# Performance work log

Measured on AMD Instinct MI355X. Metric: run time of the kernel, lower is better.

## Reference

```python
import jax, jax.numpy as jnp
import numpy as np

N_NODES = 50000
NEG_SLOPE = 0.2


def gat_conv(x, edge_index, W, a_src, a_dst, b):
    """PyG GATConv, heads=1: linear -> per-edge attention -> segment softmax -> scatter-add."""
    n = x.shape[0]
    h = x @ W                                   # [N, out]
    # add self-loops (PyG default add_self_loops=True)
    loop = jnp.arange(n, dtype=edge_index.dtype)
    src = jnp.concatenate([edge_index[0], loop])  # message sources j
    dst = jnp.concatenate([edge_index[1], loop])  # aggregation targets i
    alpha_s = h @ a_src                          # [N]
    alpha_d = h @ a_dst                          # [N]
    e = jax.nn.leaky_relu(alpha_s[src] + alpha_d[dst], NEG_SLOPE)  # [E+N]
    # numerically stable segment softmax over edges grouped by dst
    m = jax.ops.segment_max(e, dst, num_segments=n)
    ex = jnp.exp(e - m[dst])
    denom = jax.ops.segment_sum(ex, dst, num_segments=n)
    alpha = ex / denom[dst]                      # [E+N]
    out = jax.ops.segment_sum(h[src] * alpha[:, None], dst, num_segments=n)
    return out + b


def setup_inputs() -> dict:
    key = jax.random.key(0)
    ks = jax.random.split(key, 12)
    F_IN, H1, H2 = 128, 64, 32
    E, ED = 800000, 800000
    x = jax.random.normal(ks[0], (N_NODES, F_IN), dtype=jnp.float32)
    edge_index = jax.random.randint(ks[1], (2, E), 0, N_NODES, dtype=jnp.int64)
    pos_edge_index = jax.random.randint(ks[2], (2, ED), 0, N_NODES, dtype=jnp.int64)
    neg_edge_index = jax.random.randint(ks[3], (2, ED), 0, N_NODES, dtype=jnp.int64)
    g = lambda k, shape, fan: (jax.random.normal(k, shape, dtype=jnp.float32) * (1.0 / np.sqrt(fan))).astype(jnp.float32)
    W1 = g(ks[4], (F_IN, H1), F_IN)
    a_src1 = g(ks[5], (H1,), H1)
    a_dst1 = g(ks[6], (H1,), H1)
    b1 = jnp.zeros((H1,), dtype=jnp.float32)
    W2 = g(ks[7], (H1, H2), H1)
    a_src2 = g(ks[8], (H2,), H2)
    a_dst2 = g(ks[9], (H2,), H2)
    b2 = jnp.zeros((H2,), dtype=jnp.float32)
    return {"x": x, "edge_index": edge_index, "pos_edge_index": pos_edge_index,
            "neg_edge_index": neg_edge_index, "W1": W1, "a_src1": a_src1,
            "a_dst1": a_dst1, "b1": b1, "W2": W2, "a_src2": a_src2,
            "a_dst2": a_dst2, "b2": b2}


def reference(x, edge_index, pos_edge_index, neg_edge_index,
              W1, a_src1, a_dst1, b1, W2, a_src2, a_dst2, b2):
    # encode (dropout omitted: eval-mode)
    h = gat_conv(x, edge_index, W1, a_src1, a_dst1, b1)
    h = jax.nn.relu(h)
    z = gat_conv(h, edge_index, W2, a_src2, a_dst2, b2)
    # decode: per-edge dot products on concatenated pos/neg edges
    ei = jnp.concatenate([pos_edge_index, neg_edge_index], axis=-1)
    logits = jnp.sum(z[ei[0]] * z[ei[1]], axis=-1)
    return logits
```

## Files before the change

kernel.cpp:

```cpp
#include <hip/hip_runtime.h>

#define NEG_SLOPE 0.2f

constexpr int N_NODES = 50000;
constexpr int TPB = 256;
constexpr int BSH = 7;
constexpr int NB = (N_NODES + 127) >> BSH;
constexpr int SCAT_CHUNK = 8192;

__device__ __forceinline__ unsigned short f2b(float f) {
  unsigned u = __float_as_uint(f);
  return (unsigned short)((u + 0x7FFFu + ((u >> 16) & 1u)) >> 16);
}
__device__ __forceinline__ float b2f(unsigned short b) {
  return __uint_as_float(((unsigned)b) << 16);
}
__device__ __forceinline__ float blo(unsigned u) {
  return __uint_as_float(u << 16);
}
__device__ __forceinline__ float bhi(unsigned u) {
  return __uint_as_float(u & 0xFFFF0000u);
}
__device__ __forceinline__ unsigned pack2(float a, float b) {
  return (unsigned)f2b(a) | ((unsigned)f2b(b) << 16);
}

__global__ void zero_ints(int* __restrict__ p, int n) {
  int i = blockIdx.x * blockDim.x + threadIdx.x;
  if (i < n) p[i] = 0;
}

__global__ void transpose_w4(const float* __restrict__ W,
                             float4* __restrict__ Wt, int K, int OUTD) {
  int i = blockIdx.x * blockDim.x + threadIdx.x;
  if (i >= (K / 4) * OUTD) return;
  int k4 = i / OUTD, c = i % OUTD;
  Wt[i] = make_float4(W[(4 * k4 + 0) * OUTD + c], W[(4 * k4 + 1) * OUTD + c],
                      W[(4 * k4 + 2) * OUTD + c], W[(4 * k4 + 3) * OUTD + c]);
}

template <int K, int OUTD>
__global__ __launch_bounds__(TPB) void gemm_alpha(
    const float* __restrict__ X, const float4* __restrict__ Wt,
    const float* __restrict__ avec_src, const float* __restrict__ avec_dst,
    unsigned short* __restrict__ Hout, float* __restrict__ as_out,
    float* __restrict__ ad_out, int n) {
  constexpr int BK = 16;
  constexpr int NT = K / BK;
  constexpr int CT = OUTD / 2;
  constexpr int RG = 64 / CT;
  constexpr int RPT = 16 / RG;
  constexpr int WPB = TPB / 64;
  __shared__ float xs[WPB][2][16][BK + 4];

  const int t = threadIdx.x;
  const int wid = t >> 6;
  const int lane = t & 63;
  const int waveRow0 = blockIdx.x * (WPB * 16) + wid * 16;

  const int srow = lane >> 2;
  const int skq = lane & 3;
  const float* srcRow = X + (size_t)min(waveRow0 + srow, n - 1) * K + skq * 4;

  const int cc = lane % CT;
  const int c0 = 2 * cc;
  const int rg = lane / CT;
  const int r0 = rg * RPT;

  const float a_s0 = avec_src[c0], a_s1 = avec_src[c0 + 1];
  const float a_d0 = avec_dst[c0], a_d1 = avec_dst[c0 + 1];

  float4 g = *(const float4*)srcRow;
  *(float4*)&xs[wid][0][srow][skq * 4] = g;

  float acc[RPT][2];
#pragma unroll
  for (int i = 0; i < RPT; ++i) acc[i][0] = acc[i][1] = 0.f;

  for (int tile = 0;;) {
    if (tile + 1 < NT)
      g = *(const float4*)(srcRow + (size_t)(tile + 1) * BK);
    const int buf = tile & 1;
#pragma unroll
    for (int kq = 0; kq < BK / 4; ++kq) {
      const int kqg = tile * (BK / 4) + kq;
      const float4 w0 = Wt[(size_t)kqg * OUTD + c0];
      const float4 w1 = Wt[(size_t)kqg * OUTD + c0 + 1];
#pragma unroll
      for (int i = 0; i < RPT; ++i) {
        const float4 xv = *(const float4*)&xs[wid][buf][r0 + i][kq * 4];
        acc[i][0] = fmaf(xv.x, w0.x, acc[i][0]);
        acc[i][1] = fmaf(xv.x, w1.x, acc[i][1]);
        acc[i][0] = fmaf(xv.y, w0.y, acc[i][0]);
        acc[i][1] = fmaf(xv.y, w1.y, acc[i][1]);
        acc[i][0] = fmaf(xv.z, w0.z, acc[i][0]);
        acc[i][1] = fmaf(xv.z, w1.z, acc[i][1]);
        acc[i][0] = fmaf(xv.w, w0.w, acc[i][0]);
        acc[i][1] = fmaf(xv.w, w1.w, acc[i][1]);
      }
    }
    if (++tile == NT) break;
    *(float4*)&xs[wid][tile & 1][srow][skq * 4] = g;
  }

#pragma unroll
  for (int i = 0; i < RPT; ++i) {
    const int r = waveRow0 + r0 + i;
    if (r < n) {
      ushort2 hb;
      hb.x = f2b(acc[i][0]);
      hb.y = f2b(acc[i][1]);
      ((ushort2*)Hout)[(size_t)r * CT + cc] = hb;
      float vs = acc[i][0] * a_s0 + acc[i][1] * a_s1;
      float vd = acc[i][0] * a_d0 + acc[i][1] * a_d1;
#pragma unroll
      for (int m = CT / 2; m >= 1; m >>= 1) {
        vs += __shfl_xor(vs, m);
        vd += __shfl_xor(vd, m);
      }
      if (cc == 0) {
        as_out[r] = vs;
        ad_out[r] = vd;
      }
    }
  }
}

__global__ void bucket_hist(const int* __restrict__ edst, int E,
                            int* __restrict__ pairCnt) {
  __shared__ int h[NB];
  for (int i = threadIdx.x; i < NB; i += blockDim.x) h[i] = 0;
  __syncthreads();
  for (int i = blockIdx.x * blockDim.x + threadIdx.x; i < E;
       i += gridDim.x * blockDim.x)
    atomicAdd(&h[edst[i] >> BSH], 1);
  __syncthreads();
  for (int i = threadIdx.x; i < NB; i += blockDim.x)
    if (h[i]) atomicAdd(&pairCnt[i], h[i]);
}

__global__ void bucket_scan(const int* __restrict__ pairCnt,
                            int* __restrict__ pairOff,
                            int* __restrict__ pairCursor,
                            int* __restrict__ csrOff, int N) {
  __shared__ int a[512], b[512];
  const int t = threadIdx.x;
  const int pc = (t < NB) ? pairCnt[t] : 0;
  const int nodes = (t < NB) ? min(128, N - (t << BSH)) : 0;
  a[t] = pc;
  b[t] = pc + nodes;
  __syncthreads();
  for (int off = 1; off < 512; off <<= 1) {
    int av = (t >= off) ? a[t - off] : 0;
    int bv = (t >= off) ? b[t - off] : 0;
    __syncthreads();
    a[t] += av;
    b[t] += bv;
    __syncthreads();
  }
  if (t < NB) {
    const int pe = a[t] - pc;
    pairOff[t] = pe;
    pairCursor[t] = pe;
    csrOff[t] = b[t] - (pc + nodes);
  }
  if (t == 0) {
    pairOff[NB] = a[511];
    csrOff[NB] = b[511];
  }
}

__global__ void bucket_scatter(const int* __restrict__ esrc,
                               const int* __restrict__ edst, int E,
                               int* __restrict__ pairCursor,
                               unsigned* __restrict__ stage) {
  __shared__ int h[NB], baseA[NB];
  const int base0 = blockIdx.x * SCAT_CHUNK;
  const int lim = min(E, base0 + SCAT_CHUNK);
  for (int i = threadIdx.x; i < NB; i += blockDim.x) h[i] = 0;
  __syncthreads();
  for (int i = base0 + threadIdx.x; i < lim; i += blockDim.x)
    atomicAdd(&h[edst[i] >> BSH], 1);
  __syncthreads();
  for (int i = threadIdx.x; i < NB; i += blockDim.x) {
    const int c = h[i];
    baseA[i] = c ? atomicAdd(&pairCursor[i], c) : 0;
  }
  __syncthreads();
  for (int i = threadIdx.x; i < NB; i += blockDim.x) h[i] = 0;
  __syncthreads();
  for (int i = base0 + threadIdx.x; i < lim; i += blockDim.x) {
    const int d = edst[i];
    const int s = esrc[i];
    const int bkt = d >> BSH;
    const int pos = baseA[bkt] + atomicAdd(&h[bkt], 1);
    stage[pos] = ((unsigned)(d & 127) << 16) | (unsigned)s;
  }
}

__global__ void build_csr(const unsigned* __restrict__ stage,
                          const int* __restrict__ pairOff,
                          const int* __restrict__ csrOff, int N,
                          int* __restrict__ rowoff, int* __restrict__ psrc) {
  __shared__ int cnt[128], excl[128];
  const int b = blockIdx.x, t = threadIdx.x;
  const int n0 = b << BSH;
  const int nn = min(128, N - n0);
  if (t < 128) cnt[t] = (t < nn) ? 1 : 0;
  __syncthreads();
  const int pb = pairOff[b], pe = pairOff[b + 1];
  for (int k = pb + t; k < pe; k += blockDim.x)
    atomicAdd(&cnt[stage[k] >> 16], 1);
  __syncthreads();
  if (t < 128) excl[t] = cnt[t];
  __syncthreads();
  for (int off = 1; off < 128; off <<= 1) {
    int v = (t < 128 && t >= off) ? excl[t - off] : 0;
    __syncthreads();
    if (t < 128) excl[t] += v;
    __syncthreads();
  }
  const int cb = csrOff[b];
  if (t < 128) {
    const int ex = excl[t] - cnt[t];
    if (t < nn) {
      rowoff[n0 + t] = cb + ex;
      psrc[cb + ex] = n0 + t;
    }
    cnt[t] = ex + 1;
  }
  if (b == 0 && t == 0) rowoff[N] = csrOff[NB];
  __syncthreads();
  for (int k = pb + t; k < pe; k += blockDim.x) {
    const unsigned p = stage[k];
    const int ld = p >> 16;
    const int s = p & 0xFFFF;
    const int pos = cb + atomicAdd(&cnt[ld], 1);
    psrc[pos] = s;
  }
}

template <int D, bool OUT_BF16>
__global__ __launch_bounds__(TPB) void gat_aggregate(
    const unsigned short* __restrict__ Hb, const float* __restrict__ as,
    const float* __restrict__ ad, const int* __restrict__ rowoff,
    const int* __restrict__ psrc, int n, const float* __restrict__ bias,
    float* __restrict__ outF, unsigned short* __restrict__ outB, int doRelu) {
  constexpr int LPE = D / 4;
  constexpr int EPS = 64 / LPE;
  constexpr int WPB = TPB / 64;
  __shared__ float2 wsP[WPB][64];

  const int wave = (blockIdx.x * blockDim.x + threadIdx.x) >> 6;
  const int wid = threadIdx.x >> 6;
  const int lane = threadIdx.x & 63;
  if (wave >= n) return;
  const int i = wave;
  const int beg = rowoff[i];
  const int end = rowoff[i + 1];
  const float adi = ad[i];

  const int p = lane / LPE;
  const int fl4 = (lane % LPE) * 4;

  float m = -1e30f, denom = 0.f;
  float4 acc = make_float4(0.f, 0.f, 0.f, 0.f);

  for (int c = beg; c < end; c += 64) {
    const int k = c + lane;
    const bool valid = (k < end);
    int s = 0;
    float e = -1e30f;
    if (valid) {
      s = psrc[k];
      e = as[s] + adi;
      e = (e > 0.f) ? e : e * NEG_SLOPE;
    }
    float cm = e;
#pragma unroll
    for (int mm = 32; mm >= 1; mm >>= 1) cm = fmaxf(cm, __shfl_xor(cm, mm));
    const float nm = fmaxf(m, cm);
    const float scale = __expf(m - nm);
    const float w = valid ? __expf(e - nm) : 0.f;
    float ws = w;
#pragma unroll
    for (int mm = 32; mm >= 1; mm >>= 1) ws += __shfl_xor(ws, mm);
    denom = denom * scale + ws;
    acc.x *= scale;
    acc.y *= scale;
    acc.z *= scale;
    acc.w *= scale;
    m = nm;

    wsP[wid][lane] = make_float2(w, __int_as_float(s));

    const int cnt = min(64, end - c);
    const int nsteps = (cnt + EPS - 1) / EPS;
#pragma unroll 4
    for (int j = 0; j < nsteps; ++j) {
      const float2 p2 = wsP[wid][j * EPS + p];
      const float wj = p2.x;
      const int sj = __float_as_int(p2.y);
      const ushort4 hu = *(const ushort4*)(Hb + (size_t)sj * D + fl4);
      acc.x = fmaf(wj, b2f(hu.x), acc.x);
      acc.y = fmaf(wj, b2f(hu.y), acc.y);
      acc.z = fmaf(wj, b2f(hu.z), acc.z);
      acc.w = fmaf(wj, b2f(hu.w), acc.w);
    }
  }
#pragma unroll
  for (int mm = LPE; mm < 64; mm <<= 1) {
    acc.x += __shfl_xor(acc.x, mm);
    acc.y += __shfl_xor(acc.y, mm);
    acc.z += __shfl_xor(acc.z, mm);
    acc.w += __shfl_xor(acc.w, mm);
  }
  if (lane < LPE) {
    const float4 bv = *(const float4*)(bias + fl4);
    float4 o;
    o.x = acc.x / denom + bv.x;
    o.y = acc.y / denom + bv.y;
    o.z = acc.z / denom + bv.z;
    o.w = acc.w / denom + bv.w;
    if (doRelu) {
      o.x = fmaxf(o.x, 0.f);
      o.y = fmaxf(o.y, 0.f);
      o.z = fmaxf(o.z, 0.f);
      o.w = fmaxf(o.w, 0.f);
    }
    if (OUT_BF16) {
      ushort4 ob;
      ob.x = f2b(o.x);
      ob.y = f2b(o.y);
      ob.z = f2b(o.z);
      ob.w = f2b(o.w);
      *(ushort4*)(outB + (size_t)i * D + fl4) = ob;
    } else {
      *(float4*)(outF + (size_t)i * D + fl4) = o;
    }
  }
}

__device__ __forceinline__ int loadS(const int* __restrict__ pos,
                                     const int* __restrict__ neg, int ED,
                                     int g) {
  return (g < ED) ? pos[g] : neg[g - ED];
}
__device__ __forceinline__ int loadD(const int* __restrict__ pos,
                                     const int* __restrict__ neg, int ED,
                                     int g) {
  return (g < ED) ? pos[ED + g] : neg[ED + (g - ED)];
}

__global__ __launch_bounds__(TPB) void decode_kernel(
    const unsigned short* __restrict__ zb, const int* __restrict__ pos,
    const int* __restrict__ neg, int ED, float* __restrict__ out) {
  const int wv = (blockIdx.x * blockDim.x + threadIdx.x) >> 6;
  const int lane = threadIdx.x & 63;
  const int g0 = wv * 16;
  const int NG = 2 * ED;
  if (g0 >= NG) return;

  int my = 0;
  if (lane < 32) {
    const int g = g0 + (lane & 15);
    if (g < NG)
      my = (lane < 16) ? loadS(pos, neg, ED, g) : loadD(pos, neg, ED, g);
  }
  const int e = lane >> 2;
  const int fl = lane & 3;
  const int s = __shfl(my, e);
  const int d = __shfl(my, 16 + e);
  const int g = g0 + e;
  if (g >= NG) return;

  const uint4 a = ((const uint4*)(zb + (size_t)s * 32))[fl];
  const uint4 b = ((const uint4*)(zb + (size_t)d * 32))[fl];
  float v = blo(a.x) * blo(b.x) + bhi(a.x) * bhi(b.x);
  v = fmaf(blo(a.y), blo(b.y), v);
  v = fmaf(bhi(a.y), bhi(b.y), v);
  v = fmaf(blo(a.z), blo(b.z), v);
  v = fmaf(bhi(a.z), bhi(b.z), v);
  v = fmaf(blo(a.w), blo(b.w), v);
  v = fmaf(bhi(a.w), bhi(b.w), v);
  v += __shfl_xor(v, 1);
  v += __shfl_xor(v, 2);
  if (fl == 0) out[g] = v;
}

extern "C" void kernel_launch(void* const* d_in, const int* in_sizes, int n_in,
                              void* d_out, int out_size, void* d_ws,
                              size_t ws_size, hipStream_t stream) {
  const int N = N_NODES;
  const float* x = (const float*)d_in[0];
  const int* ei = (const int*)d_in[1];
  const int* pe = (const int*)d_in[2];
  const int* ne = (const int*)d_in[3];
  const float* W1 = (const float*)d_in[4];
  const float* a_src1 = (const float*)d_in[5];
  const float* a_dst1 = (const float*)d_in[6];
  const float* b1 = (const float*)d_in[7];
  const float* W2 = (const float*)d_in[8];
  const float* a_src2 = (const float*)d_in[9];
  const float* a_dst2 = (const float*)d_in[10];
  const float* b2 = (const float*)d_in[11];
  float* out = (float*)d_out;

  const int E = in_sizes[1] / 2;
  const int ED = in_sizes[2] / 2;
  const int* esrc = ei;
  const int* edst = ei + E;

  char* base = (char*)d_ws;
  size_t off = 0;
  auto alloc = [&](size_t bytes) {
    char* p = base + off;
    off = (off + bytes + 255) & ~(size_t)255;
    return p;
  };
  unsigned short* h1b = (unsigned short*)alloc((size_t)N * 64 * 2);
  float* out1 = (float*)alloc((size_t)N * 64 * 4);
  unsigned short* h2b = (unsigned short*)alloc((size_t)N * 32 * 2);
  unsigned short* zb = (unsigned short*)alloc((size_t)N * 32 * 2);
  float* as1 = (float*)alloc((size_t)N * 4);
  float* ad1 = (float*)alloc((size_t)N * 4);
  float* as2 = (float*)alloc((size_t)N * 4);
  float* ad2 = (float*)alloc((size_t)N * 4);
  int* rowoff = (int*)alloc((size_t)(N + 1) * 4);
  int* psrc = (int*)alloc((size_t)(E + N) * 4);
  unsigned* stage = (unsigned*)alloc((size_t)E * 4);
  int* pairCnt = (int*)alloc((size_t)NB * 4);
  int* pairOff = (int*)alloc((size_t)(NB + 1) * 4);
  int* pairCursor = (int*)alloc((size_t)NB * 4);
  int* csrOff = (int*)alloc((size_t)(NB + 1) * 4);
  float4* Wt1 = (float4*)alloc((size_t)(128 / 4) * 64 * 16);
  float4* Wt2 = (float4*)alloc((size_t)(64 / 4) * 32 * 16);

  zero_ints<<<(NB + 511) / 512, 512, 0, stream>>>(pairCnt, NB);
  transpose_w4<<<(32 * 64 + TPB - 1) / TPB, TPB, 0, stream>>>(W1, Wt1, 128, 64);
  transpose_w4<<<(16 * 32 + TPB - 1) / TPB, TPB, 0, stream>>>(W2, Wt2, 64, 32);

  bucket_hist<<<256, TPB, 0, stream>>>(edst, E, pairCnt);
  bucket_scan<<<1, 512, 0, stream>>>(pairCnt, pairOff, pairCursor, csrOff, N);
  bucket_scatter<<<(E + SCAT_CHUNK - 1) / SCAT_CHUNK, TPB, 0, stream>>>(
      esrc, edst, E, pairCursor, stage);
  build_csr<<<NB, TPB, 0, stream>>>(stage, pairOff, csrOff, N, rowoff, psrc);

  gemm_alpha<128, 64><<<(N + 63) / 64, TPB, 0, stream>>>(
      x, Wt1, a_src1, a_dst1, h1b, as1, ad1, N);
  gat_aggregate<64, false><<<(N + 3) / 4, TPB, 0, stream>>>(
      h1b, as1, ad1, rowoff, psrc, N, b1, out1, nullptr, 1);

  gemm_alpha<64, 32><<<(N + 63) / 64, TPB, 0, stream>>>(
      out1, Wt2, a_src2, a_dst2, h2b, as2, ad2, N);
  gat_aggregate<32, true><<<(N + 3) / 4, TPB, 0, stream>>>(
      h2b, as2, ad2, rowoff, psrc, N, b2, nullptr, zb, 0);

  const int waves = (2 * ED + 15) / 16;
  decode_kernel<<<(waves * 64 + TPB - 1) / TPB, TPB, 0, stream>>>(
      zb, pe, ne, ED, out);
}
```

Baseline: 167.2 us.

## Fuse layer-2 linear into layer-1 aggregation and merge setup kernels

Merges the weight transposes and counter zeroing into one prep kernel. The bucket histogram now runs as extra blocks of the first GEMM launch, so it overlaps with that GEMM. The second-layer GEMM and attention-logit computation are folded into the epilogue of the first aggregation, which removes the fp32 out1 round trip through memory and one launch. In exchange, the aggregation kernel does extra per-node work and the GEMM kernel carries more shared memory.

```diff
diff --git a/kernel.cpp b/kernel.cpp
--- a/kernel.cpp
+++ b/kernel.cpp
@@ -25,26 +25,36 @@
   return (unsigned)f2b(a) | ((unsigned)f2b(b) << 16);
 }
 
-__global__ void zero_ints(int* __restrict__ p, int n) {
-  int i = blockIdx.x * blockDim.x + threadIdx.x;
-  if (i < n) p[i] = 0;
-}
-
-__global__ void transpose_w4(const float* __restrict__ W,
-                             float4* __restrict__ Wt, int K, int OUTD) {
-  int i = blockIdx.x * blockDim.x + threadIdx.x;
-  if (i >= (K / 4) * OUTD) return;
+__device__ __forceinline__ void tw_elem(const float* __restrict__ W,
+                                        float4* __restrict__ Wt, int OUTD,
+                                        int i) {
   int k4 = i / OUTD, c = i % OUTD;
   Wt[i] = make_float4(W[(4 * k4 + 0) * OUTD + c], W[(4 * k4 + 1) * OUTD + c],
                       W[(4 * k4 + 2) * OUTD + c], W[(4 * k4 + 3) * OUTD + c]);
 }
 
+__global__ void prep_kernel(const float* __restrict__ W1,
+                            float4* __restrict__ Wt1,
+                            const float* __restrict__ W2,
+                            float4* __restrict__ Wt2,
+                            int* __restrict__ pairCnt) {
+  int i = blockIdx.x * blockDim.x + threadIdx.x;
+  if (i < 2048) {
+    tw_elem(W1, Wt1, 64, i);
+  } else if (i < 2048 + 512) {
+    tw_elem(W2, Wt2, 32, i - 2048);
+  } else if (i < 2048 + 512 + NB) {
+    pairCnt[i - 2560] = 0;
+  }
+}
+
 template <int K, int OUTD>
-__global__ __launch_bounds__(TPB) void gemm_alpha(
+__global__ __launch_bounds__(TPB) void gemm_alpha_hist(
     const float* __restrict__ X, const float4* __restrict__ Wt,
     const float* __restrict__ avec_src, const float* __restrict__ avec_dst,
     unsigned short* __restrict__ Hout, float* __restrict__ as_out,
-    float* __restrict__ ad_out, int n) {
+    float* __restrict__ ad_out, int n, const int* __restrict__ edst, int E,
+    int* __restrict__ pairCnt, int gemmBlocks) {
   constexpr int BK = 16;
   constexpr int NT = K / BK;
   constexpr int CT = OUTD / 2;
@@ -52,6 +62,19 @@
   constexpr int RPT = 16 / RG;
   constexpr int WPB = TPB / 64;
   __shared__ float xs[WPB][2][16][BK + 4];
+  __shared__ int hh[NB];
+
+  if (blockIdx.x >= gemmBlocks) {
+    const int vb = blockIdx.x - gemmBlocks;
+    for (int i = threadIdx.x; i < NB; i += TPB) hh[i] = 0;
+    __syncthreads();
+    for (int i = vb * TPB + threadIdx.x; i < E; i += 256 * TPB)
+      atomicAdd(&hh[edst[i] >> BSH], 1);
+    __syncthreads();
+    for (int i = threadIdx.x; i < NB; i += TPB)
+      if (hh[i]) atomicAdd(&pairCnt[i], hh[i]);
+    return;
+  }
 
   const int t = threadIdx.x;
   const int wid = t >> 6;
@@ -126,19 +149,6 @@
   }
 }
 
-__global__ void bucket_hist(const int* __restrict__ edst, int E,
-                            int* __restrict__ pairCnt) {
-  __shared__ int h[NB];
-  for (int i = threadIdx.x; i < NB; i += blockDim.x) h[i] = 0;
-  __syncthreads();
-  for (int i = blockIdx.x * blockDim.x + threadIdx.x; i < E;
-       i += gridDim.x * blockDim.x)
-    atomicAdd(&h[edst[i] >> BSH], 1);
-  __syncthreads();
-  for (int i = threadIdx.x; i < NB; i += blockDim.x)
-    if (h[i]) atomicAdd(&pairCnt[i], h[i]);
-}
-
 __global__ void bucket_scan(const int* __restrict__ pairCnt,
                             int* __restrict__ pairOff,
                             int* __restrict__ pairCursor,
@@ -240,12 +250,14 @@
   }
 }
 
-template <int D, bool OUT_BF16>
-__global__ __launch_bounds__(TPB) void gat_aggregate(
+__global__ __launch_bounds__(TPB) void gat_aggregate_fused(
     const unsigned short* __restrict__ Hb, const float* __restrict__ as,
     const float* __restrict__ ad, const int* __restrict__ rowoff,
     const int* __restrict__ psrc, int n, const float* __restrict__ bias,
-    float* __restrict__ outF, unsigned short* __restrict__ outB, int doRelu) {
+    const float4* __restrict__ Wt2, const float* __restrict__ a_src2,
+    const float* __restrict__ a_dst2, unsigned short* __restrict__ h2out,
+    float* __restrict__ as2, float* __restrict__ ad2) {
+  constexpr int D = 64;
   constexpr int LPE = D / 4;
   constexpr int EPS = 64 / LPE;
   constexpr int WPB = TPB / 64;
@@ -315,29 +327,129 @@
     acc.z += __shfl_xor(acc.z, mm);
     acc.w += __shfl_xor(acc.w, mm);
   }
+  const float4 bv = *(const float4*)(bias + fl4);
+  float4 o;
+  o.x = fmaxf(acc.x / denom + bv.x, 0.f);
+  o.y = fmaxf(acc.y / denom + bv.y, 0.f);
+  o.z = fmaxf(acc.z / denom + bv.z, 0.f);
+  o.w = fmaxf(acc.w / denom + bv.w, 0.f);
+
+  float* lrow = (float*)(&wsP[wid][0]);
+  if (lane < 16) *(float4*)(lrow + fl4) = o;
+
+  const int col = lane & 31;
+  const int half = lane >> 5;
+  float hc = 0.f;
+#pragma unroll
+  for (int j = 0; j < 8; ++j) {
+    const float4 xv = *(const float4*)(lrow + half * 32 + j * 4);
+    const float4 wv = Wt2[(size_t)(half * 8 + j) * 32 + col];
+    hc = fmaf(xv.x, wv.x, hc);
+    hc = fmaf(xv.y, wv.y, hc);
+    hc = fmaf(xv.z, wv.z, hc);
+    hc = fmaf(xv.w, wv.w, hc);
+  }
+  hc += __shfl_xor(hc, 32);
+
+  float vs = hc * a_src2[col];
+  float vd = hc * a_dst2[col];
+#pragma unroll
+  for (int mm = 16; mm >= 1; mm >>= 1) {
+    vs += __shfl_xor(vs, mm);
+    vd += __shfl_xor(vd, mm);
+  }
+  if (lane == 0) {
+    as2[i] = vs;
+    ad2[i] = vd;
+  }
+  const float hn = __shfl_xor(hc, 1);
+  if (lane < 32 && !(col & 1))
+    ((unsigned*)h2out)[(size_t)i * 16 + (col >> 1)] = pack2(hc, hn);
+}
+
+__global__ __launch_bounds__(TPB) void gat_aggregate32(
+    const unsigned short* __restrict__ Hb, const float* __restrict__ as,
+    const float* __restrict__ ad, const int* __restrict__ rowoff,
+    const int* __restrict__ psrc, int n, const float* __restrict__ bias,
+    unsigned short* __restrict__ outB) {
+  constexpr int D = 32;
+  constexpr int LPE = D / 4;
+  constexpr int EPS = 64 / LPE;
+  constexpr int WPB = TPB / 64;
+  __shared__ float2 wsP[WPB][64];
+
+  const int wave = (blockIdx.x * blockDim.x + threadIdx.x) >> 6;
+  const int wid = threadIdx.x >> 6;
+  const int lane = threadIdx.x & 63;
+  if (wave >= n) return;
+  const int i = wave;
+  const int beg = rowoff[i];
+  const int end = rowoff[i + 1];
+  const float adi = ad[i];
+
+  const int p = lane / LPE;
+  const int fl4 = (lane % LPE) * 4;
+
+  float m = -1e30f, denom = 0.f;
+  float4 acc = make_float4(0.f, 0.f, 0.f, 0.f);
+
+  for (int c = beg; c < end; c += 64) {
+    const int k = c + lane;
+    const bool valid = (k < end);
+    int s = 0;
+    float e = -1e30f;
+    if (valid) {
+      s = psrc[k];
+      e = as[s] + adi;
+      e = (e > 0.f) ? e : e * NEG_SLOPE;
+    }
+    float cm = e;
+#pragma unroll
+    for (int mm = 32; mm >= 1; mm >>= 1) cm = fmaxf(cm, __shfl_xor(cm, mm));
+    const float nm = fmaxf(m, cm);
+    const float scale = __expf(m - nm);
+    const float w = valid ? __expf(e - nm) : 0.f;
+    float ws = w;
+#pragma unroll
+    for (int mm = 32; mm >= 1; mm >>= 1) ws += __shfl_xor(ws, mm);
+    denom = denom * scale + ws;
+    acc.x *= scale;
+    acc.y *= scale;
+    acc.z *= scale;
+    acc.w *= scale;
+    m = nm;
+
+    wsP[wid][lane] = make_float2(w, __int_as_float(s));
+
+    const int cnt = min(64, end - c);
+    const int nsteps = (cnt + EPS - 1) / EPS;
+#pragma unroll 4
+    for (int j = 0; j < nsteps; ++j) {
+      const float2 p2 = wsP[wid][j * EPS + p];
+      const float wj = p2.x;
+      const int sj = __float_as_int(p2.y);
+      const ushort4 hu = *(const ushort4*)(Hb + (size_t)sj * D + fl4);
+      acc.x = fmaf(wj, b2f(hu.x), acc.x);
+      acc.y = fmaf(wj, b2f(hu.y), acc.y);
+      acc.z = fmaf(wj, b2f(hu.z), acc.z);
+      acc.w = fmaf(wj, b2f(hu.w), acc.w);
+    }
+  }
+#pragma unroll
+  for (int mm = LPE; mm < 64; mm <<= 1) {
+    acc.x += __shfl_xor(acc.x, mm);
+    acc.y += __shfl_xor(acc.y, mm);
+    acc.z += __shfl_xor(acc.z, mm);
+    acc.w += __shfl_xor(acc.w, mm);
+  }
   if (lane < LPE) {
     const float4 bv = *(const float4*)(bias + fl4);
-    float4 o;
-    o.x = acc.x / denom + bv.x;
-    o.y = acc.y / denom + bv.y;
-    o.z = acc.z / denom + bv.z;
-    o.w = acc.w / denom + bv.w;
-    if (doRelu) {
-      o.x = fmaxf(o.x, 0.f);
-      o.y = fmaxf(o.y, 0.f);
-      o.z = fmaxf(o.z, 0.f);
-      o.w = fmaxf(o.w, 0.f);
-    }
-    if (OUT_BF16) {
-      ushort4 ob;
-      ob.x = f2b(o.x);
-      ob.y = f2b(o.y);
-      ob.z = f2b(o.z);
-      ob.w = f2b(o.w);
-      *(ushort4*)(outB + (size_t)i * D + fl4) = ob;
-    } else {
-      *(float4*)(outF + (size_t)i * D + fl4) = o;
-    }
+    ushort4 ob;
+    ob.x = f2b(acc.x / denom + bv.x);
+    ob.y = f2b(acc.y / denom + bv.y);
+    ob.z = f2b(acc.z / denom + bv.z);
+    ob.w = f2b(acc.w / denom + bv.w);
+    *(ushort4*)(outB + (size_t)i * D + fl4) = ob;
   }
 }
 
@@ -419,7 +531,6 @@
     return p;
   };
   unsigned short* h1b = (unsigned short*)alloc((size_t)N * 64 * 2);
-  float* out1 = (float*)alloc((size_t)N * 64 * 4);
   unsigned short* h2b = (unsigned short*)alloc((size_t)N * 32 * 2);
   unsigned short* zb = (unsigned short*)alloc((size_t)N * 32 * 2);
   float* as1 = (float*)alloc((size_t)N * 4);
@@ -436,25 +547,23 @@
   float4* Wt1 = (float4*)alloc((size_t)(128 / 4) * 64 * 16);
   float4* Wt2 = (float4*)alloc((size_t)(64 / 4) * 32 * 16);
 
-  zero_ints<<<(NB + 511) / 512, 512, 0, stream>>>(pairCnt, NB);
-  transpose_w4<<<(32 * 64 + TPB - 1) / TPB, TPB, 0, stream>>>(W1, Wt1, 128, 64);
-  transpose_w4<<<(16 * 32 + TPB - 1) / TPB, TPB, 0, stream>>>(W2, Wt2, 64, 32);
-
-  bucket_hist<<<256, TPB, 0, stream>>>(edst, E, pairCnt);
+  prep_kernel<<<(2048 + 512 + NB + TPB - 1) / TPB, TPB, 0, stream>>>(
+      W1, Wt1, W2, Wt2, pairCnt);
+
+  const int gemmBlocks = (N + 63) / 64;
+  gemm_alpha_hist<128, 64><<<gemmBlocks + 256, TPB, 0, stream>>>(
+      x, Wt1, a_src1, a_dst1, h1b, as1, ad1, N, edst, E, pairCnt, gemmBlocks);
+
   bucket_scan<<<1, 512, 0, stream>>>(pairCnt, pairOff, pairCursor, csrOff, N);
   bucket_scatter<<<(E + SCAT_CHUNK - 1) / SCAT_CHUNK, TPB, 0, stream>>>(
       esrc, edst, E, pairCursor, stage);
   build_csr<<<NB, TPB, 0, stream>>>(stage, pairOff, csrOff, N, rowoff, psrc);
 
-  gemm_alpha<128, 64><<<(N + 63) / 64, TPB, 0, stream>>>(
-      x, Wt1, a_src1, a_dst1, h1b, as1, ad1, N);
-  gat_aggregate<64, false><<<(N + 3) / 4, TPB, 0, stream>>>(
-      h1b, as1, ad1, rowoff, psrc, N, b1, out1, nullptr, 1);
-
-  gemm_alpha<64, 32><<<(N + 63) / 64, TPB, 0, stream>>>(
-      out1, Wt2, a_src2, a_dst2, h2b, as2, ad2, N);
-  gat_aggregate<32, true><<<(N + 3) / 4, TPB, 0, stream>>>(
-      h2b, as2, ad2, rowoff, psrc, N, b2, nullptr, zb, 0);
+  gat_aggregate_fused<<<(N + 3) / 4, TPB, 0, stream>>>(
+      h1b, as1, ad1, rowoff, psrc, N, b1, Wt2, a_src2, a_dst2, h2b, as2, ad2);
+
+  gat_aggregate32<<<(N + 3) / 4, TPB, 0, stream>>>(h2b, as2, ad2, rowoff, psrc,
+                                                   N, b2, zb);
 
   const int waves = (2 * ED + 15) / 16;
   decode_kernel<<<(waves * 64 + TPB - 1) / TPB, TPB, 0, stream>>>(
```

Result: faster. 147.1 us (-12.0%).
